# Performance work log

Measured on AMD Instinct MI355X. Metric: run time of the kernel, lower is better.

Reference implementation:

```python
import jax, jax.numpy as jnp
import numpy as np

B, T, DIM = 4, 1024, 2048
N_HEADS, N_KV_HEADS = 32, 8
HEAD_DIM = DIM // N_HEADS  # 64
N_REPS = N_HEADS // N_KV_HEADS  # 4


def setup_inputs() -> dict:
    key = jax.random.key(0)
    ks = jax.random.split(key, 8)
    # RoPE tables: theta = 10000^{-2i/d}, positions 0..T-1
    inv_freq = 1.0 / (10000.0 ** (jnp.arange(0, HEAD_DIM, 2, dtype=jnp.float32) / HEAD_DIM))
    angles = jnp.arange(T, dtype=jnp.float32)[:, None] * inv_freq[None, :]  # (T, HEAD_DIM//2)
    s = 0.02
    return {
        "input": jax.random.normal(ks[0], (B, T, DIM), jnp.float32),
        "freqs_cos": jnp.cos(angles),
        "freqs_sin": jnp.sin(angles),
        "mask": jnp.tril(jnp.ones((T, T), dtype=bool)),  # causal boolean mask
        "wq": s * jax.random.normal(ks[1], (DIM, DIM), jnp.float32),
        "wk": s * jax.random.normal(ks[2], (N_KV_HEADS * HEAD_DIM, DIM), jnp.float32),
        "wv": s * jax.random.normal(ks[3], (N_KV_HEADS * HEAD_DIM, DIM), jnp.float32),
        "wo": s * jax.random.normal(ks[4], (DIM, DIM), jnp.float32),
        "curr_pos": 0,
    }


def _apply_rope(x, cos, sin):
    # x: (B, T, H, D); cos/sin: (T, D//2). Complex multiply on (even, odd) pairs.
    xr = x[..., 0::2]
    xi = x[..., 1::2]
    c = cos[None, :, None, :]
    s = sin[None, :, None, :]
    out_r = xr * c - xi * s
    out_i = xr * s + xi * c
    return jnp.stack([out_r, out_i], axis=-1).reshape(x.shape)


def reference(input, freqs_cos, freqs_sin, mask, wq, wk, wv, wo, curr_pos):
    Bv, Tv = input.shape[0], input.shape[1]
    qs = (input @ wq.T).reshape(Bv, Tv, N_HEADS, HEAD_DIM)
    ks = (input @ wk.T).reshape(Bv, Tv, N_KV_HEADS, HEAD_DIM)
    vs = (input @ wv.T).reshape(Bv, Tv, N_KV_HEADS, HEAD_DIM)
    qs = _apply_rope(qs, freqs_cos, freqs_sin)
    ks = _apply_rope(ks, freqs_cos, freqs_sin)

    # KV cache (prefill path: curr_pos == 0, fresh cache of length 2T)
    kv_cache = jnp.zeros((Bv, 2 * Tv, N_KV_HEADS, HEAD_DIM, 2), input.dtype)
    kv_cache = kv_cache.at[:, curr_pos:curr_pos + Tv, :, :, 0].set(ks)
    kv_cache = kv_cache.at[:, curr_pos:curr_pos + Tv, :, :, 1].set(vs)
    k_all = kv_cache[:, :curr_pos + Tv, :, :, 0]
    v_all = kv_cache[:, :curr_pos + Tv, :, :, 1]

    # GQA: broadcast each kv head across its query-head group (avoid repeat_interleave copy)
    S = k_all.shape[1]
    q = qs.transpose(0, 2, 1, 3).reshape(Bv, N_KV_HEADS, N_REPS, Tv, HEAD_DIM)
    k = k_all.transpose(0, 2, 1, 3)  # (B, KVH, S, D)
    v = v_all.transpose(0, 2, 1, 3)

    scale = 1.0 / jnp.sqrt(jnp.asarray(HEAD_DIM, input.dtype))
    scores = jnp.einsum("bgrqd,bgkd->bgrqk", q, k) * scale  # (B, KVH, REPS, T, S)
    neg = jnp.asarray(jnp.finfo(input.dtype).min, input.dtype)
    scores = jnp.where(mask[None, None, None, :, :S], scores, neg)
    attn = jax.nn.softmax(scores, axis=-1)
    out = jnp.einsum("bgrqk,bgkd->bgrqd", attn, v)
    out = out.reshape(Bv, N_HEADS, Tv, HEAD_DIM).transpose(0, 2, 1, 3).reshape(Bv, Tv, DIM)
    return out @ wo.T
```

## Files before the change

kernel.cpp:

```cpp
#include <hip/hip_runtime.h>
#include <cstdint>

typedef __bf16 bf16x8 __attribute__((ext_vector_type(8)));
typedef float  f32x4  __attribute__((ext_vector_type(4)));
typedef float  f32x16 __attribute__((ext_vector_type(16)));
typedef float  float8v __attribute__((ext_vector_type(8)));
typedef unsigned short ushort8v __attribute__((ext_vector_type(8)));
typedef unsigned short ushort4v __attribute__((ext_vector_type(4)));
typedef unsigned int   uint4v   __attribute__((ext_vector_type(4)));

__device__ __forceinline__ unsigned short f2b(float f) {
  uint32_t u = __builtin_bit_cast(uint32_t, f);
  u += 0x7FFFu + ((u >> 16) & 1u);
  return (unsigned short)(u >> 16);
}
__device__ __forceinline__ float b2f(unsigned short h) {
  uint32_t u = ((uint32_t)h) << 16;
  return __builtin_bit_cast(float, u);
}
__device__ __forceinline__ unsigned int cvtpk(float lo, float hi_) {
  unsigned int r;
  asm("v_cvt_pk_bf16_f32 %0, %1, %2" : "=v"(r) : "v"(lo), "v"(hi_));
  return r;
}

__device__ __forceinline__ void async16(const void* g, void* l) {
  __builtin_amdgcn_global_load_lds(
      (const __attribute__((address_space(1))) void*)g,
      (__attribute__((address_space(3))) void*)l, 16, 0, 0);
}

#define WAITVM(N)  __builtin_amdgcn_s_waitcnt(0x0F70 | ((N) & 15))

struct CvtArgs {
  const float* src[5];
  unsigned short* dst[5];
  long n[5];
};
__global__ void cvt5_kernel(CvtArgs a) {
  long base = (long)blockIdx.x * blockDim.x + threadIdx.x;
  long gstride = (long)gridDim.x * blockDim.x;
#pragma unroll 1
  for (int sg = 0; sg < 5; ++sg) {
    const float* s = a.src[sg];
    unsigned short* d = a.dst[sg];
    long n8 = a.n[sg] >> 3;
    for (long i = base; i < n8; i += gstride) {
      float8v f = *(const float8v*)(s + i * 8);
      ushort8v o;
#pragma unroll
      for (int j = 0; j < 8; ++j) o[j] = f2b(f[j]);
      *(ushort8v*)(d + i * 8) = o;
    }
  }
}

template<bool F32OUT, int BN, int GX, int GY>
__global__ __launch_bounds__(512, 2)
void gemm8p(const unsigned short* __restrict__ Ag, const unsigned short* __restrict__ Wg,
            void* __restrict__ Cp, int N) {
  constexpr int K = 2048;
  constexpr int BM = 256;
  constexpr int NF = BN / 64;
  constexpr int AL = 2;
  constexpr int BL = BN / 128;
  constexpr int VMS = 2 * BL + AL;
  constexpr int ASLOT = BM * 64;
  constexpr int BSLOT = BN * 64;
  constexpr int NWG = GX * GY;
  constexpr int CPX = NWG / 8;

  extern __shared__ char lds_c[];

  const int tid = threadIdx.x;
  const int wave = tid >> 6, lane = tid & 63;
  const int wm = wave >> 2, wn = wave & 3;
  const int lr = lane & 15, lg = lane >> 4;

  const int flat = blockIdx.y * GX + blockIdx.x;
  const int swz = (flat & 7) * CPX + (flat >> 3);
  const int m0 = (swz / GX) * BM, n0 = (swz % GX) * BN;

  const int laneSw = (lr >> 1) * 128 + (((((lr & 1) << 2) | lg) ^ (lr >> 1)) << 4);
  const int aoff = wm * 128 * 64 + laneSw;
  const int boff = wn * NF * 1024 + laneSw;

  f32x4 acc[8][NF] = {};
  bf16x8 af[4], bf[NF];

  auto stA = [&](int slot, int s) {
    char* sl = lds_c + slot * ASLOT;
    const int kc = s * 32;
#pragma unroll
    for (int j = 0; j < AL; ++j) {
      int q = (tid + 512 * j) * 16;
      int R = q >> 7, g2L = ((q >> 4) & 7) ^ (R & 7);
      int row = R * 2 + (g2L >> 2), kg = g2L & 3;
      async16(Ag + (size_t)(m0 + row) * K + kc + kg * 8, sl + q);
    }
  };
  auto stB = [&](int slot, int s) {
    char* sl = lds_c + 4 * ASLOT + slot * BSLOT;
    const int kc = s * 32;
#pragma unroll
    for (int j = 0; j < BL; ++j) {
      int q = (tid + 512 * j) * 16;
      int R = q >> 7, g2L = ((q >> 4) & 7) ^ (R & 7);
      int row = R * 2 + (g2L >> 2), kg = g2L & 3;
      async16(Wg + (size_t)(n0 + row) * K + kc + kg * 8, sl + q);
    }
  };

#define PH(RSLOT, MH, RDB, STG, VM)                                           \
  {                                                                           \
    const char* As_ = lds_c + (RSLOT) * ASLOT;                                \
    _Pragma("unroll") for (int mi = 0; mi < 4; ++mi)                          \
      af[mi] = *(const bf16x8*)(As_ + aoff + ((MH) * 4 + mi) * 1024);         \
    if (RDB) {                                                                \
      const char* Bs_ = lds_c + 4 * ASLOT + (RSLOT) * BSLOT;                  \
      _Pragma("unroll") for (int ni = 0; ni < NF; ++ni)                       \
        bf[ni] = *(const bf16x8*)(Bs_ + boff + ni * 1024);                    \
    }                                                                         \
    STG;                                                                      \
    if ((VM) >= 0) WAITVM(VM);                                                \
    __builtin_amdgcn_s_barrier();                                             \
    __builtin_amdgcn_s_setprio(1);                                            \
    _Pragma("unroll") for (int mi = 0; mi < 4; ++mi)                          \
      _Pragma("unroll") for (int ni = 0; ni < NF; ++ni)                       \
        acc[(MH) * 4 + mi][ni] = __builtin_amdgcn_mfma_f32_16x16x32_bf16(     \
            af[mi], bf[ni], acc[(MH) * 4 + mi][ni], 0, 0, 0);                 \
    __builtin_amdgcn_s_setprio(0);                                            \
    __builtin_amdgcn_s_barrier();                                             \
  }

  stB(0, 0); stA(0, 0); stB(1, 1); stA(1, 1); stB(2, 2); stA(2, 2); stB(3, 3);
  WAITVM(VMS);
  __builtin_amdgcn_s_barrier();

  for (int T = 0; T < 30; T += 2) {
    const int p0 = 2 * T;
    PH(0, 0, true,  stA(3, p0 + 3), -1);
    PH(0, 1, false, stB(0, p0 + 4), -1);
    PH(1, 0, true,  stA(0, p0 + 4), -1);
    PH(1, 1, false, stB(1, p0 + 5), VMS);
    PH(2, 0, true,  stA(1, p0 + 5), -1);
    PH(2, 1, false, stB(2, p0 + 6), -1);
    PH(3, 0, true,  stA(2, p0 + 6), -1);
    PH(3, 1, false, stB(3, p0 + 7), VMS);
  }
  PH(0, 0, true,  stA(3, 63), -1);
  PH(0, 1, false, (void)0, -1);
  PH(1, 0, true,  (void)0, -1);
  PH(1, 1, false, (void)0, 0);
  PH(2, 0, true,  (void)0, -1);
  PH(2, 1, false, (void)0, -1);
  PH(3, 0, true,  (void)0, -1);
  PH(3, 1, false, (void)0, -1);
#undef PH

#pragma unroll
  for (int mig = 0; mig < 8; ++mig) {
#pragma unroll
    for (int j = 0; j < 4; ++j) {
      int row = m0 + wm * 128 + mig * 16 + lg * 4 + j;
#pragma unroll
      for (int ni = 0; ni < NF; ++ni) {
        int col = n0 + wn * (NF * 16) + ni * 16 + lr;
        float v = acc[mig][ni][j];
        if (F32OUT) ((float*)Cp)[(size_t)row * N + col] = v;
        else        ((unsigned short*)Cp)[(size_t)row * N + col] = f2b(v);
      }
    }
  }
}

__global__ __launch_bounds__(256)
void ropekv_kernel(unsigned short* __restrict__ qkv,
                   const float* __restrict__ cosb, const float* __restrict__ sinb,
                   unsigned short* __restrict__ vt) {
  const int tt0 = blockIdx.x * 64;
  const int kvh = blockIdx.y;
  const int b   = blockIdx.z;
  const int tid = threadIdx.x;

  {
    int r = tid >> 2, c0 = (tid & 3) * 16;
    int t = tt0 + r;
    unsigned short* kp = qkv + (size_t)(b * 1024 + t) * 3072 + 2048 + kvh * 64 + c0;
    const float* cb = cosb + t * 32 + c0 / 2;
    const float* sb = sinb + t * 32 + c0 / 2;
    ushort8v x0 = *(const ushort8v*)kp;
    ushort8v x1 = *(const ushort8v*)(kp + 8);
    float8v c = *(const float8v*)cb;
    float8v s = *(const float8v*)sb;
    ushort8v o0, o1;
#pragma unroll
    for (int j = 0; j < 4; ++j) {
      float xr = b2f(x0[2 * j]), xi = b2f(x0[2 * j + 1]);
      o0[2 * j]     = f2b(xr * c[j] - xi * s[j]);
      o0[2 * j + 1] = f2b(xr * s[j] + xi * c[j]);
    }
#pragma unroll
    for (int j = 0; j < 4; ++j) {
      float xr = b2f(x1[2 * j]), xi = b2f(x1[2 * j + 1]);
      o1[2 * j]     = f2b(xr * c[4 + j] - xi * s[4 + j]);
      o1[2 * j + 1] = f2b(xr * s[4 + j] + xi * c[4 + j]);
    }
    *(ushort8v*)kp = o0;
    *(ushort8v*)(kp + 8) = o1;
  }

  __shared__ unsigned short lT[64 * 68];
#pragma unroll
  for (int i = 0; i < 2; ++i) {
    int r = i * 32 + (tid >> 3), c = (tid & 7) * 8;
    const unsigned short* src = qkv + (size_t)(b * 1024 + tt0 + r) * 3072 + 2560 + kvh * 64 + c;
    ushort8v v = *(const ushort8v*)src;
    ushort4v a, b4;
#pragma unroll
    for (int j = 0; j < 4; ++j) { a[j] = v[j]; b4[j] = v[j + 4]; }
    *(ushort4v*)&lT[r * 68 + c]     = a;
    *(ushort4v*)&lT[r * 68 + c + 4] = b4;
  }
  __syncthreads();
#pragma unroll
  for (int i = 0; i < 2; ++i) {
    int d = tid & 63;
    int tt = i * 4 + (tid >> 6);
    ushort8v o;
#pragma unroll
    for (int j = 0; j < 8; ++j) o[j] = lT[(tt * 8 + j) * 68 + d];
    *(ushort8v*)&vt[((size_t)((b * 8 + kvh) * 64 + d)) * 1024 + tt0 + tt * 8] = o;
  }
}

__global__ __launch_bounds__(256, 2)
void attn_kernel(const unsigned short* __restrict__ qkv, const unsigned short* __restrict__ vt,
                 const float* __restrict__ cosb, const float* __restrict__ sinb,
                 unsigned short* __restrict__ ob) {
  const int flat = (blockIdx.z * 8 + blockIdx.y) * 16 + blockIdx.x;
  const int swzb = (flat & 7) * 64 + (flat >> 3);
  const int bx = swzb & 15, kvh = (swzb >> 4) & 7, b = swzb >> 7;

  const int tid = threadIdx.x, wave = tid >> 6, lane = tid & 63;
  const int l31 = lane & 31, hi = lane >> 5;
  const int h = kvh * 4 + wave;

  const int qth = 31 - bx, qtl = bx;
  const int q0h = qth * 32, q0l = qtl * 32;
  const int nth = qth / 4 + 1, ntl = qtl / 4 + 1;
  const int ntot = nth + ntl;

  __shared__ unsigned short lK[2][128 * 64];
  __shared__ unsigned short lVt[2][64 * 128];

  auto ldq = [&](int q0, bf16x8* qf) {
    int t = q0 + l31;
    const unsigned short* qp = qkv + (size_t)(b * 1024 + t) * 3072 + h * 64;
#pragma unroll
    for (int dk = 0; dk < 4; ++dk) {
      ushort8v q = *(const ushort8v*)(qp + dk * 16 + hi * 8);
      f32x4 c4 = *(const f32x4*)(cosb + t * 32 + dk * 8 + hi * 4);
      f32x4 s4 = *(const f32x4*)(sinb + t * 32 + dk * 8 + hi * 4);
      ushort8v o;
#pragma unroll
      for (int j = 0; j < 4; ++j) {
        float xr = b2f(q[2 * j]), xi = b2f(q[2 * j + 1]);
        o[2 * j]     = f2b(xr * c4[j] - xi * s4[j]);
        o[2 * j + 1] = f2b(xr * s4[j] + xi * c4[j]);
      }
      qf[dk] = __builtin_bit_cast(bf16x8, o);
    }
  };

  const unsigned short* kg = qkv + (size_t)(b * 1024) * 3072 + 2048 + kvh * 64;
  const unsigned short* vg = vt + (size_t)(b * 8 + kvh) * 64 * 1024;

  auto stage = [&](int kvb, int bi) {
    const int sr  = tid >> 3;
    const int scb = (tid & 7) * 16;
#pragma unroll
    for (int i = 0; i < 4; ++i) {
      int r = i * 32 + sr;
      int cb = scb ^ ((r & 7) << 4);
      async16(kg + (size_t)(kvb + r) * 3072 + (cb >> 1), &lK[bi][r * 64 + (scb >> 1)]);
    }
    const int rv0 = tid >> 4;
    const int scv = (tid & 15) * 16;
#pragma unroll
    for (int i = 0; i < 4; ++i) {
      int rv = i * 16 + rv0;
      int cbv = scv ^ ((rv & 15) << 4);
      async16(vg + (size_t)rv * 1024 + kvb + (cbv >> 1), &lVt[bi][rv * 128 + (scv >> 1)]);
    }
  };

  bf16x8 qf[4];
  f32x16 oacc[2] = {};
  float m2 = -3e38f, l_run = 0.f;
  int q0 = q0h;

  ldq(q0h, qf);

  const float SC = 0.125f * 1.44269504f;

  auto chunk64 = [&](int cur, int ckvb, int c, bool lastT) {
    f32x16 sd[2] = {};
    __builtin_amdgcn_s_setprio(1);
#pragma unroll
    for (int s = 0; s < 2; ++s) {
      const int krow = c * 64 + s * 32 + l31;
      const char* kr = (const char*)lK[cur] + krow * 128;
      const int swz = (krow & 7) << 4;
#pragma unroll
      for (int dk = 0; dk < 4; ++dk) {
        bf16x8 kf = *(const bf16x8*)(kr + ((dk * 32 + hi * 16) ^ swz));
        sd[s] = __builtin_amdgcn_mfma_f32_32x32x16_bf16(kf, qf[dk], sd[s], 0, 0, 0);
      }
    }
    __builtin_amdgcn_s_setprio(0);

#pragma unroll
    for (int s = 0; s < 2; ++s)
#pragma unroll
      for (int r = 0; r < 16; ++r) {
        float v = sd[s][r] * SC;
        if (lastT) {
          int kvg = ckvb + s * 32 + (r & 3) + 8 * (r >> 2) + 4 * hi;
          if (kvg > q0 + l31) v = -3e38f;
        }
        sd[s][r] = v;
      }
    float pm = sd[0][0];
#pragma unroll
    for (int s = 0; s < 2; ++s)
#pragma unroll
      for (int r = 0; r < 16; ++r) pm = fmaxf(pm, sd[s][r]);
    pm = fmaxf(pm, __shfl_xor(pm, 32));
    if (!__all(pm <= m2 + 11.0f)) {
      float mnew = fmaxf(m2, pm);
      float alpha = exp2f(m2 - mnew);
      m2 = mnew;
      l_run *= alpha;
#pragma unroll
      for (int db = 0; db < 2; ++db)
#pragma unroll
        for (int r = 0; r < 16; ++r) oacc[db][r] *= alpha;
    }
    float tsum = 0.f;
#pragma unroll
    for (int s = 0; s < 2; ++s)
#pragma unroll
      for (int r = 0; r < 16; ++r) { float p = exp2f(sd[s][r] - m2); sd[s][r] = p; tsum += p; }
    tsum += __shfl_xor(tsum, 32);
    l_run += tsum;

    bf16x8 pf[2][2];
#pragma unroll
    for (int s = 0; s < 2; ++s)
#pragma unroll
      for (int kc = 0; kc < 2; ++kc) {
        unsigned int cA = cvtpk(sd[s][8 * kc + 0], sd[s][8 * kc + 1]);
        unsigned int cB = cvtpk(sd[s][8 * kc + 4], sd[s][8 * kc + 5]);
        unsigned int cC = cvtpk(sd[s][8 * kc + 2], sd[s][8 * kc + 3]);
        unsigned int cD = cvtpk(sd[s][8 * kc + 6], sd[s][8 * kc + 7]);
        unsigned int xA = __shfl_xor(cA, 32), xB = __shfl_xor(cB, 32);
        unsigned int xC = __shfl_xor(cC, 32), xD = __shfl_xor(cD, 32);
        uint4v u;
        u[0] = hi ? xB : cA;
        u[1] = hi ? xD : cC;
        u[2] = hi ? cB : xA;
        u[3] = hi ? cD : xC;
        pf[s][kc] = __builtin_bit_cast(bf16x8, u);
      }

    __builtin_amdgcn_s_setprio(1);
#pragma unroll
    for (int db = 0; db < 2; ++db) {
      const int row = db * 32 + l31;
      const char* vr = (const char*)lVt[cur] + row * 256;
      const int vswz = (row & 15) << 4;
#pragma unroll
      for (int s = 0; s < 2; ++s)
#pragma unroll
        for (int kc = 0; kc < 2; ++kc) {
          bf16x8 vf = *(const bf16x8*)(vr + ((c * 128 + s * 64 + kc * 32 + hi * 16) ^ vswz));
          oacc[db] = __builtin_amdgcn_mfma_f32_32x32x16_bf16(vf, pf[s][kc], oacc[db], 0, 0, 0);
        }
    }
    __builtin_amdgcn_s_setprio(0);
  };

  auto writeOut = [&](int q0w) {
    float inv = 1.0f / l_run;
    unsigned short* orow = ob + (size_t)(b * 1024 + q0w + l31) * 2048 + h * 64;
#pragma unroll
    for (int db = 0; db < 2; ++db)
#pragma unroll
      for (int g = 0; g < 4; ++g) {
        int d0 = db * 32 + 8 * g + 4 * hi;
        ushort4v o;
#pragma unroll
        for (int j = 0; j < 4; ++j) o[j] = f2b(oacc[db][4 * g + j] * inv);
        *(ushort4v*)(orow + d0) = o;
      }
  };

  auto kvb_of = [&](int j) { return (j < nth ? j : j - nth) * 128; };

  stage(0, 0);
  __syncthreads();

  for (int j = 0; j < ntot; ++j) {
    const int cur = j & 1;
    if (j + 1 < ntot) stage(kvb_of(j + 1), cur ^ 1);
    const int kvb = kvb_of(j);
    const bool lastT = (j == nth - 1) || (j == ntot - 1);

#pragma unroll 1
    for (int c = 0; c < 2; ++c) {
      if (kvb + c * 64 > q0 + 31) continue;
      chunk64(cur, kvb + c * 64, c, lastT);
    }

    if (j == nth - 1) {
      writeOut(q0h);
      oacc[0] = f32x16{}; oacc[1] = f32x16{};
      m2 = -3e38f; l_run = 0.f;
      q0 = q0l;
      ldq(q0l, qf);
    }
    __syncthreads();
  }
  writeOut(q0l);
}

extern "C" void kernel_launch(void* const* d_in, const int* in_sizes, int n_in,
                              void* d_out, int out_size, void* d_ws, size_t ws_size,
                              hipStream_t stream) {
  const float* input = (const float*)d_in[0];
  const float* fcos  = (const float*)d_in[1];
  const float* fsin  = (const float*)d_in[2];
  const float* wq = (const float*)d_in[4];
  const float* wk = (const float*)d_in[5];
  const float* wv = (const float*)d_in[6];
  const float* wo = (const float*)d_in[7];
  float* out = (float*)d_out;

  unsigned short* xb   = (unsigned short*)d_ws;
  unsigned short* wqkv = xb + (size_t)4096 * 2048;
  unsigned short* wob  = wqkv + (size_t)3072 * 2048;
  unsigned short* qkv  = wob + (size_t)2048 * 2048;
  unsigned short* ob   = qkv + (size_t)4096 * 3072;
  unsigned short* vtb  = xb;

  hipFuncSetAttribute((const void*)&gemm8p<false, 256, 12, 16>,
                      hipFuncAttributeMaxDynamicSharedMemorySize, 131072);
  hipFuncSetAttribute((const void*)&gemm8p<true, 128, 16, 16>,
                      hipFuncAttributeMaxDynamicSharedMemorySize, 98304);

  CvtArgs ca;
  ca.src[0] = input; ca.dst[0] = xb;                        ca.n[0] = (long)4096 * 2048;
  ca.src[1] = wq;    ca.dst[1] = wqkv;                      ca.n[1] = (long)2048 * 2048;
  ca.src[2] = wk;    ca.dst[2] = wqkv + (size_t)2048 * 2048; ca.n[2] = (long)512 * 2048;
  ca.src[3] = wv;    ca.dst[3] = wqkv + (size_t)2560 * 2048; ca.n[3] = (long)512 * 2048;
  ca.src[4] = wo;    ca.dst[4] = wob;                       ca.n[4] = (long)2048 * 2048;
  hipLaunchKernelGGL(cvt5_kernel, dim3(2048), dim3(256), 0, stream, ca);

  hipLaunchKernelGGL((gemm8p<false, 256, 12, 16>), dim3(12, 16), dim3(512), 131072,
                     stream, xb, wqkv, (void*)qkv, 3072);

  hipLaunchKernelGGL(ropekv_kernel, dim3(16, 8, 4), dim3(256), 0, stream,
                     qkv, fcos, fsin, vtb);

  hipLaunchKernelGGL(attn_kernel, dim3(16, 8, 4), dim3(256), 0, stream,
                     qkv, vtb, fcos, fsin, ob);

  hipLaunchKernelGGL((gemm8p<true, 128, 16, 16>), dim3(16, 16), dim3(512), 98304,
                     stream, ob, wob, (void*)out, 2048);
}
```

Measured before the change: 168.3 us.

## Replace QKV projection GEMM with dedicated 256x192-tile kernel

Adds a specialized QKV GEMM kernel that uses 256x192 output tiles, giving a 16x16 grid of 256 workgroups instead of 12x16 with 256-wide tiles. It has its own software pipeline: four A stages of 32-wide K slices and two B stages of 64-wide K slices, with swizzled LDS layouts and a remapped block order. The aim is to fill all compute units evenly and cut LDS use so occupancy improves. The cost is a hand-scheduled phase sequence and a scalar bf16 store epilogue that may coalesce poorly.

```diff
diff --git a/kernel.cpp b/kernel.cpp
--- a/kernel.cpp
+++ b/kernel.cpp
@@ -51,6 +51,123 @@
 #pragma unroll
       for (int j = 0; j < 8; ++j) o[j] = f2b(f[j]);
       *(ushort8v*)(d + i * 8) = o;
+    }
+  }
+}
+
+__global__ __launch_bounds__(512, 2)
+void gemmQ192(const unsigned short* __restrict__ Ag, const unsigned short* __restrict__ Wg,
+              unsigned short* __restrict__ Cp) {
+  constexpr int K = 2048;
+  constexpr int NF = 3;
+  constexpr int ASLOT = 16384;
+  constexpr int BSLOT = 24576;
+  constexpr int N = 3072;
+
+  extern __shared__ char lds_c[];
+
+  const int tid = threadIdx.x;
+  const int wave = tid >> 6, lane = tid & 63;
+  const int wm = wave >> 2, wn = wave & 3;
+  const int lr = lane & 15, lg = lane >> 4;
+
+  const int flat = blockIdx.y * 16 + blockIdx.x;
+  const int swz = (flat & 7) * 32 + (flat >> 3);
+  const int m0 = (swz >> 4) * 256, n0 = (swz & 15) * 192;
+
+  const int laneSw = (lr >> 1) * 128 + (((((lr & 1) << 2) | lg) ^ (lr >> 1)) << 4);
+  const int aoff = wm * 8192 + laneSw;
+
+  int bByte[NF], bR7[NF];
+#pragma unroll
+  for (int ni = 0; ni < NF; ++ni) {
+    int row = wn * 48 + ni * 16 + lr;
+    bByte[ni] = row * 128;
+    bR7[ni] = row & 7;
+  }
+
+  f32x4 acc[8][NF] = {};
+  bf16x8 af[4], bf[NF];
+
+  auto stA = [&](int slot, int s) {
+    char* sl = lds_c + slot * ASLOT;
+    const int kc = s * 32;
+#pragma unroll
+    for (int j = 0; j < 2; ++j) {
+      int q = (tid + 512 * j) * 16;
+      int R = q >> 7, g2L = ((q >> 4) & 7) ^ (R & 7);
+      int row = R * 2 + (g2L >> 2), kg = g2L & 3;
+      async16(Ag + (size_t)(m0 + row) * K + kc + kg * 8, sl + q);
+    }
+  };
+  auto stB = [&](int slot, int T) {
+    char* sl = lds_c + 4 * ASLOT + slot * BSLOT;
+    const int kc = T * 64;
+#pragma unroll
+    for (int j = 0; j < 3; ++j) {
+      int q = (tid + 512 * j) * 16;
+      int row = q >> 7, c = (q >> 4) & 7;
+      async16(Wg + (size_t)(n0 + row) * K + kc + ((c ^ (row & 7)) * 8), sl + q);
+    }
+  };
+
+#define PH(SA, SB, MH, KH, RDB, STG, VM)                                      \
+  {                                                                           \
+    const char* As_ = lds_c + (SA) * ASLOT;                                   \
+    _Pragma("unroll") for (int mi = 0; mi < 4; ++mi)                          \
+      af[mi] = *(const bf16x8*)(As_ + aoff + ((MH) * 4 + mi) * 1024);         \
+    if (RDB) {                                                                \
+      const char* Bs_ = lds_c + 4 * ASLOT + (SB) * BSLOT;                     \
+      _Pragma("unroll") for (int ni = 0; ni < NF; ++ni)                       \
+        bf[ni] = *(const bf16x8*)(Bs_ + bByte[ni] +                           \
+                                  (((((KH) << 2) | lg) ^ bR7[ni]) << 4));     \
+    }                                                                         \
+    STG;                                                                      \
+    if ((VM) >= 0) WAITVM(VM);                                                \
+    __builtin_amdgcn_s_barrier();                                             \
+    __builtin_amdgcn_s_setprio(1);                                            \
+    _Pragma("unroll") for (int mi = 0; mi < 4; ++mi)                          \
+      _Pragma("unroll") for (int ni = 0; ni < NF; ++ni)                       \
+        acc[(MH) * 4 + mi][ni] = __builtin_amdgcn_mfma_f32_16x16x32_bf16(     \
+            af[mi], bf[ni], acc[(MH) * 4 + mi][ni], 0, 0, 0);                 \
+    __builtin_amdgcn_s_setprio(0);                                            \
+    __builtin_amdgcn_s_barrier();                                             \
+  }
+
+  stB(0, 0); stA(0, 0); stA(1, 1); stB(1, 1); stA(2, 2);
+  WAITVM(5);
+  __builtin_amdgcn_s_barrier();
+
+  for (int t2 = 0; t2 < 30; t2 += 2) {
+    PH(0, 0, 0, 0, true,  stA(3, 2 * t2 + 3), -1);
+    PH(0, 0, 1, 0, false, (void)0, -1);
+    PH(1, 0, 0, 1, true,  stA(0, 2 * t2 + 4), -1);
+    PH(1, 0, 1, 1, false, stB(0, t2 + 2), 5);
+    PH(2, 1, 0, 0, true,  stA(1, 2 * t2 + 5), -1);
+    PH(2, 1, 1, 0, false, (void)0, -1);
+    PH(3, 1, 0, 1, true,  stA(2, 2 * t2 + 6), -1);
+    PH(3, 1, 1, 1, false, stB(1, t2 + 3), 5);
+  }
+  PH(0, 0, 0, 0, true,  stA(3, 63), -1);
+  PH(0, 0, 1, 0, false, (void)0, -1);
+  PH(1, 0, 0, 1, true,  (void)0, -1);
+  PH(1, 0, 1, 1, false, (void)0, 0);
+  PH(2, 1, 0, 0, true,  (void)0, -1);
+  PH(2, 1, 1, 0, false, (void)0, -1);
+  PH(3, 1, 0, 1, true,  (void)0, -1);
+  PH(3, 1, 1, 1, false, (void)0, -1);
+#undef PH
+
+#pragma unroll
+  for (int mig = 0; mig < 8; ++mig) {
+#pragma unroll
+    for (int j = 0; j < 4; ++j) {
+      int row = m0 + wm * 128 + mig * 16 + lg * 4 + j;
+#pragma unroll
+      for (int ni = 0; ni < NF; ++ni) {
+        int col = n0 + wn * 48 + ni * 16 + lr;
+        Cp[(size_t)row * N + col] = f2b(acc[mig][ni][j]);
+      }
     }
   }
 }
@@ -454,8 +571,8 @@
   unsigned short* ob   = qkv + (size_t)4096 * 3072;
   unsigned short* vtb  = xb;
 
-  hipFuncSetAttribute((const void*)&gemm8p<false, 256, 12, 16>,
-                      hipFuncAttributeMaxDynamicSharedMemorySize, 131072);
+  hipFuncSetAttribute((const void*)&gemmQ192,
+                      hipFuncAttributeMaxDynamicSharedMemorySize, 114688);
   hipFuncSetAttribute((const void*)&gemm8p<true, 128, 16, 16>,
                       hipFuncAttributeMaxDynamicSharedMemorySize, 98304);
 
@@ -467,8 +584,8 @@
   ca.src[4] = wo;    ca.dst[4] = wob;                       ca.n[4] = (long)2048 * 2048;
   hipLaunchKernelGGL(cvt5_kernel, dim3(2048), dim3(256), 0, stream, ca);
 
-  hipLaunchKernelGGL((gemm8p<false, 256, 12, 16>), dim3(12, 16), dim3(512), 131072,
-                     stream, xb, wqkv, (void*)qkv, 3072);
+  hipLaunchKernelGGL(gemmQ192, dim3(16, 16), dim3(512), 114688,
+                     stream, xb, wqkv, qkv);
 
   hipLaunchKernelGGL(ropekv_kernel, dim3(16, 8, 4), dim3(256), 0, stream,
                      qkv, fcos, fsin, vtb);
```

New measurement: 163.9 us. 2.6% less time.
